# Kernel tuning notes

Hardware: AMD Instinct MI355X
Metric: run time of the kernel (lower is better)

The kernel has to match this reference:

```python
import jax, jax.numpy as jnp
import numpy as np

B, S, HID = 2, 1024, 2048
H, D, KV = 32, 64, 8          # query heads, head dim, kv heads (GQA)
INNER = H * D                 # 2048
KV_DIM = KV * D               # 512


def setup_inputs() -> dict:
    key = jax.random.key(0)
    ks = jax.random.split(key, 12)
    s = 0.02
    return {
        "query": jax.random.normal(ks[0], (B, S, HID), jnp.float32),
        "key": jax.random.normal(ks[1], (B, S, HID), jnp.float32),
        "value": jax.random.normal(ks[2], (B, S, HID), jnp.float32),
        "mask": jnp.zeros((B, 1, S, S), jnp.float32),
        "position_bias": jax.random.normal(ks[3], (1, H, S, S), jnp.float32),
        "Wq": jax.random.normal(ks[4], (HID, INNER), jnp.float32) * s,
        "bq": jnp.zeros((INNER,), jnp.float32),
        "Wk": jax.random.normal(ks[5], (HID, KV_DIM), jnp.float32) * s,
        "bk": jnp.zeros((KV_DIM,), jnp.float32),
        "Wv": jax.random.normal(ks[6], (HID, KV_DIM), jnp.float32) * s,
        "bv": jnp.zeros((KV_DIM,), jnp.float32),
        "Wo": jax.random.normal(ks[7], (INNER, HID), jnp.float32) * s,
        "bo": jnp.zeros((HID,), jnp.float32),
    }


def reference(query, key, value, mask, position_bias, Wq, bq, Wk, bk, Wv, bv, Wo, bo):
    # projections (torch nn.Linear equivalent, weights stored [in,out])
    q = (query @ Wq + bq).reshape(B, S, H, D)     # [B,S,H,D]
    k = (key @ Wk + bk).reshape(B, S, KV, D)      # [B,S,KV,D]
    v = (value @ Wv + bv).reshape(B, S, KV, D)
    rep = H // KV
    k = jnp.repeat(k, rep, axis=2)                # GQA repeat_kv -> [B,S,H,D]
    v = jnp.repeat(v, rep, axis=2)
    scores = jnp.einsum("bqhd,bkhd->bhqk", q, k)  # [B,H,S,S]
    scores = (scores + position_bias) * (1.0 / jnp.sqrt(jnp.float32(D)))
    scores = scores + mask
    probs = jax.nn.softmax(scores.astype(jnp.float32), axis=-1).astype(q.dtype)
    out = jnp.einsum("bhqk,bkhd->bqhd", probs, v).reshape(B, S, INNER)
    return out @ Wo + bo                          # [B,S,HID]
```

## Files before the change

### kernel.cpp

```cpp
#include <hip/hip_runtime.h>
#include <stdint.h>


#define DEVI __device__ __forceinline__

typedef __attribute__((ext_vector_type(8))) short bf16x8;
typedef __attribute__((ext_vector_type(4))) float f32x4;
typedef __attribute__((ext_vector_type(4))) float flt4;
typedef __attribute__((ext_vector_type(8))) unsigned short u16x8;
typedef __attribute__((ext_vector_type(4))) unsigned short u16x4;

DEVI unsigned short f2bf(float f){
  union{float f;uint32_t u;}v; v.f=f;
  uint32_t u=v.u;
  u += 0x7FFFu + ((u>>16)&1u);
  return (unsigned short)(u>>16);
}

DEVI uint32_t cvt_pk_bf16(float lo, float hi){
  uint32_t r;
  asm("v_cvt_pk_bf16_f32 %0, %1, %2" : "=v"(r) : "v"(lo), "v"(hi));
  return r;
}

DEVI float fexp2(float x){
#if __has_builtin(__builtin_amdgcn_exp2f)
  return __builtin_amdgcn_exp2f(x);
#else
  return exp2f(x);
#endif
}

DEVI void gload16(const void* g, void* l){
  __builtin_amdgcn_global_load_lds((const __attribute__((address_space(1))) void*)g,
                                   (__attribute__((address_space(3))) void*)l, 16, 0, 0);
}

__global__ void prep_k(const float* __restrict__ q, const float* __restrict__ k,
                       const float* __restrict__ v,
                       unsigned short* __restrict__ qb, unsigned short* __restrict__ kb,
                       unsigned short* __restrict__ vb,
                       const float* __restrict__ Wq, const float* __restrict__ Wk,
                       const float* __restrict__ Wv, const float* __restrict__ Wo,
                       unsigned short* __restrict__ WqT, unsigned short* __restrict__ WkT,
                       unsigned short* __restrict__ WvT, unsigned short* __restrict__ WoT){
  __shared__ float tile[64][65];
  int bid = blockIdx.x;
  if (bid < 6144){
    int z = bid>>11;
    int i = (bid&2047)*256 + threadIdx.x;
    const float* src = z==0 ? q : (z==1 ? k : v);
    unsigned short* dst = z==0 ? qb : (z==1 ? kb : vb);
    const flt4* s = (const flt4*)src;
    flt4 a = s[2*i], b = s[2*i+1];
    u16x8 o;
    o[0]=f2bf(a.x); o[1]=f2bf(a.y); o[2]=f2bf(a.z); o[3]=f2bf(a.w);
    o[4]=f2bf(b.x); o[5]=f2bf(b.y); o[6]=f2bf(b.z); o[7]=f2bf(b.w);
    ((u16x8*)dst)[i] = o;
    return;
  }
  int id = bid - 6144;
  const int K = 2048;
  const float* W; unsigned short* WT; int N, tt;
  if (id < 1024)      { W=Wq; WT=WqT; N=2048; tt=id; }
  else if (id < 1280) { W=Wk; WT=WkT; N=512;  tt=id-1024; }
  else if (id < 1536) { W=Wv; WT=WvT; N=512;  tt=id-1280; }
  else                { W=Wo; WT=WoT; N=2048; tt=id-1536; }
  int sh = (N==2048) ? 5 : 3;
  int n0 = (tt & ((1<<sh)-1))*64, k0 = (tt >> sh)*64;
  int t = threadIdx.x;
  int r = t>>4, c4 = (t&15)*4;
  #pragma unroll
  for (int i=0;i<4;i++){
    flt4 vv = *(const flt4*)&W[(size_t)(k0 + r + i*16)*N + n0 + c4];
    tile[r+i*16][c4+0]=vv.x; tile[r+i*16][c4+1]=vv.y; tile[r+i*16][c4+2]=vv.z; tile[r+i*16][c4+3]=vv.w;
  }
  __syncthreads();
  #pragma unroll
  for (int i=0;i<4;i++){
    int rn = r + i*16;
    u16x4 o;
    o[0]=f2bf(tile[c4+0][rn]); o[1]=f2bf(tile[c4+1][rn]);
    o[2]=f2bf(tile[c4+2][rn]); o[3]=f2bf(tile[c4+3][rn]);
    *(u16x4*)&WT[(size_t)(n0+rn)*K + k0 + c4] = o;
  }
}

#define GEMM64_KSTEP(A_, BT_, K_)                                              \
    __syncthreads();                                                           \
    _Pragma("unroll")                                                          \
    for (int j=0;j<2;j++){                                                     \
      int cid = (j*4+w)*64 + l;                                                \
      int row = cid>>3, sl = cid&7;                                            \
      int gsl = sl ^ (row&7);                                                  \
      gload16(&A_ [(size_t)(m0+row)*K_ + k0 + gsl*8], &As[(j*4+w)*512]);       \
      gload16(&BT_[(size_t)(n0+row)*K_ + k0 + gsl*8], &Bs[(j*4+w)*512]);       \
    }                                                                          \
    __syncthreads();                                                           \
    _Pragma("unroll")                                                          \
    for (int kk=0;kk<2;kk++){                                                  \
      bf16x8 af[2], bfv[2];                                                    \
      _Pragma("unroll")                                                        \
      for (int mt=0;mt<2;mt++){                                                \
        int row = wr+mt*16+lq;                                                 \
        af[mt] = *(const bf16x8*)&As[row*64 + (((kk*4+lg)^(lq&7))*8)];         \
      }                                                                        \
      _Pragma("unroll")                                                        \
      for (int nt=0;nt<2;nt++){                                                \
        int row = wc+nt*16+lq;                                                 \
        bfv[nt] = *(const bf16x8*)&Bs[row*64 + (((kk*4+lg)^(lq&7))*8)];        \
      }                                                                        \
      _Pragma("unroll")                                                        \
      for (int mt=0;mt<2;mt++)                                                 \
        _Pragma("unroll")                                                      \
        for (int nt=0;nt<2;nt++)                                               \
          acc[mt][nt] = __builtin_amdgcn_mfma_f32_16x16x32_bf16(af[mt], bfv[nt], acc[mt][nt], 0,0,0); \
    }

__global__ __launch_bounds__(256) void qkv64(const unsigned short* __restrict__ qbf,
    const unsigned short* __restrict__ kbf, const unsigned short* __restrict__ vbf,
    const unsigned short* __restrict__ WqT, const unsigned short* __restrict__ WkT,
    const unsigned short* __restrict__ WvT,
    const float* __restrict__ bq, const float* __restrict__ bk, const float* __restrict__ bv,
    unsigned short* __restrict__ Qp, unsigned short* __restrict__ Kp, unsigned short* __restrict__ VTb){
  __shared__ unsigned short As[64*64];
  __shared__ unsigned short Bs[64*64];
  const int K = 2048;
  int id = blockIdx.x;
  const unsigned short *A, *BT; const float* bias; int N, op, tt;
  if (id < 1024)      { op=0; A=qbf; BT=WqT; bias=bq; N=2048; tt=id; }
  else if (id < 1280) { op=1; A=kbf; BT=WkT; bias=bk; N=512;  tt=id-1024; }
  else                { op=2; A=vbf; BT=WvT; bias=bv; N=512;  tt=id-1280; }
  int sh = (N==2048) ? 5 : 3;
  int n0 = (tt & ((1<<sh)-1))*64, m0 = (tt >> sh)*64;
  int t = threadIdx.x, w = t>>6, l = t&63;
  int lq = l&15, lg = l>>4;
  int wr = (w>>1)*32, wc = (w&1)*32;
  f32x4 acc[2][2] = {};
  for (int k0=0;k0<K;k0+=64){
    GEMM64_KSTEP(A, BT, K)
  }
  #pragma unroll
  for (int nt=0;nt<2;nt++){
    int col = n0 + wc + nt*16 + lq;
    float bvl = bias[col];
    #pragma unroll
    for (int mt=0;mt<2;mt++){
      #pragma unroll
      for (int r=0;r<4;r++){
        int row = m0 + wr + mt*16 + lg*4 + r;
        float v = acc[mt][nt][r] + bvl;
        if (op==0)      Qp[(size_t)row*2048 + col] = f2bf(v);
        else if (op==1) Kp[(size_t)row*512 + col] = f2bf(v);
        else {
          int b = row>>10, s = row&1023;
          VTb[((size_t)(b*512 + col)<<10) + s] = f2bf(v);
        }
      }
    }
  }
}

__global__ __launch_bounds__(256) void oproj64(const unsigned short* __restrict__ A,
    const unsigned short* __restrict__ BT, const float* __restrict__ bias,
    float* __restrict__ Cout){
  __shared__ unsigned short As[64*64];
  __shared__ unsigned short Bs[64*64];
  const int K = 2048, N = 2048;
  int n0 = blockIdx.x*64, m0 = blockIdx.y*64;
  int t = threadIdx.x, w = t>>6, l = t&63;
  int lq = l&15, lg = l>>4;
  int wr = (w>>1)*32, wc = (w&1)*32;
  f32x4 acc[2][2] = {};
  for (int k0=0;k0<K;k0+=64){
    GEMM64_KSTEP(A, BT, K)
  }
  #pragma unroll
  for (int nt=0;nt<2;nt++){
    int col = n0 + wc + nt*16 + lq;
    float bvl = bias[col];
    #pragma unroll
    for (int mt=0;mt<2;mt++){
      #pragma unroll
      for (int r=0;r<4;r++){
        int row = m0 + wr + mt*16 + lg*4 + r;
        Cout[(size_t)row*N + col] = acc[mt][nt][r] + bvl;
      }
    }
  }
}

__global__ __launch_bounds__(512,2) void attn_k(const unsigned short* __restrict__ Q,
    const unsigned short* __restrict__ Kp, const unsigned short* __restrict__ VT,
    const float* __restrict__ pbias, const float* __restrict__ mask,
    unsigned short* __restrict__ Oout){
  __shared__ unsigned short Ks[2][2][2048];
  __shared__ unsigned short VTs[2][4096];
  __shared__ float Ms[2][2][1024];
  __shared__ unsigned short Pb[8][512];
  int t=threadIdx.x, w=t>>6, l=t&63;
  int kv = blockIdx.x & 7;
  int qb = blockIdx.x >> 3;
  int h = kv*4 + (w&3);
  int qhalf = w>>2;
  int lq = l&15, lg = l>>4;
  int q0 = qb*32 + qhalf*16;
  int mr = qhalf*16 + lq;
  bf16x8 qfA0, qfA1, qfB0, qfB1;
  {
    const unsigned short* qp = &Q[((size_t)(q0 + lq))*2048 + h*64 + lg*8];
    qfA0 = *(const bf16x8*)qp;  qfA1 = *(const bf16x8*)(qp + 32);
    qp += (size_t)1024*2048;
    qfB0 = *(const bf16x8*)qp;  qfB1 = *(const bf16x8*)(qp + 32);
  }
  const float* pbase = &pbias[((size_t)h*1024 + (q0+lq))*1024];
  f32x4 oaccA[4] = {}, oaccB[4] = {};
  float psumA = 0.f, psumB = 0.f;
  const float L2E   = 1.4426950408889634f;
  const float SCL2E = 0.125f*1.4426950408889634f;
  const float NFM   = -16.0f*1.4426950408889634f;
  unsigned short* pw = &Pb[w][0];
  int swz = (lq&3)<<3;

  flt4 RA[2], RB[2], comb[2][2];

#define ATTN_STAGE(buf_, kt_)                                                            \
  {                                                                                      \
    { int bb = w>>2; int row = (w&3)*8 + (l>>3); int ch = (l&7)^(row&7);                 \
      gload16(&Kp[((size_t)(bb*1024 + (kt_)*32 + row))*512 + kv*64 + ch*8],              \
              &Ks[buf_][0][0] + w*512); }                                                \
    { int row = w*8 + (l>>3); int g = (l&7)^(row&7);                                     \
      gload16(&VT[((size_t)((g>>2)*512 + kv*64 + row))*1024 + (kt_)*32 + (g&3)*8],       \
              &VTs[buf_][0] + w*512); }                                                  \
    { int bb = w>>2; int row = (w&3)*8 + (l>>3); int ch = (l&7)^(row&7);                 \
      gload16(&mask[((size_t)(bb*1024 + qb*32 + row))*1024 + (kt_)*32 + ch*4],           \
              &Ms[buf_][0][0] + w*256); }                                                \
  }

#define ATTN_RAW(RP_, kt_)                                                               \
  _Pragma("unroll")                                                                      \
  for (int nt=0;nt<2;nt++)                                                               \
    RP_[nt] = *(const flt4*)&pbase[(kt_)*32 + nt*16 + lg*4];

#define ATTN_COMBINE(RP_, cur_)                                                          \
  _Pragma("unroll")                                                                      \
  for (int bb=0;bb<2;bb++)                                                               \
    _Pragma("unroll")                                                                    \
    for (int nt=0;nt<2;nt++){                                                            \
      flt4 m4 = *(const flt4*)&Ms[cur_][bb][mr*32 + (((nt*4+lg)^(mr&7))<<2)];            \
      _Pragma("unroll")                                                                  \
      for (int r=0;r<4;r++)                                                              \
        comb[bb][nt][r] = fmaf(RP_[nt][r], SCL2E, fmaf(m4[r], L2E, NFM));                \
    }

#define COMPUTE_BATCH(P_, bb_, QF0_, QF1_, OACC_, PS_)                                   \
  {                                                                                      \
    f32x4 sacc[2] = {};                                                                  \
    __builtin_amdgcn_s_setprio(1);                                                       \
    _Pragma("unroll")                                                                    \
    for (int nt=0;nt<2;nt++){                                                            \
      int row = nt*16 + lq;                                                              \
      bf16x8 kf0 = *(const bf16x8*)&Ks[P_][bb_][row*64 + (( lg    ^ (row&7))*8)];        \
      bf16x8 kf1 = *(const bf16x8*)&Ks[P_][bb_][row*64 + (((4+lg) ^ (row&7))*8)];        \
      sacc[nt] = __builtin_amdgcn_mfma_f32_16x16x32_bf16(kf0, QF0_, sacc[nt], 0,0,0);    \
      sacc[nt] = __builtin_amdgcn_mfma_f32_16x16x32_bf16(kf1, QF1_, sacc[nt], 0,0,0);    \
    }                                                                                    \
    __builtin_amdgcn_s_setprio(0);                                                       \
    _Pragma("unroll")                                                                    \
    for (int nt=0;nt<2;nt++){                                                            \
      float p0 = fexp2(fmaf(sacc[nt][0], SCL2E, comb[bb_][nt][0]));                      \
      float p1 = fexp2(fmaf(sacc[nt][1], SCL2E, comb[bb_][nt][1]));                      \
      float p2 = fexp2(fmaf(sacc[nt][2], SCL2E, comb[bb_][nt][2]));                      \
      float p3 = fexp2(fmaf(sacc[nt][3], SCL2E, comb[bb_][nt][3]));                      \
      PS_ += (p0+p1)+(p2+p3);                                                            \
      uint2 pk;                                                                          \
      pk.x = cvt_pk_bf16(p0,p1);                                                         \
      pk.y = cvt_pk_bf16(p2,p3);                                                         \
      *(uint2*)&pw[lq*32 + ((nt*16 + lg*4) ^ swz)] = pk;                                 \
    }                                                                                    \
    {                                                                                    \
      bf16x8 pa = *(const bf16x8*)&pw[lq*32 + ((lg*8) ^ swz)];                           \
      __builtin_amdgcn_s_setprio(1);                                                     \
      _Pragma("unroll")                                                                  \
      for (int nt=0;nt<4;nt++){                                                          \
        int vrow = nt*16 + lq;                                                           \
        bf16x8 vf = *(const bf16x8*)&VTs[P_][vrow*64 + ((((bb_)*4+lg) ^ (vrow&7))*8)];   \
        OACC_[nt] = __builtin_amdgcn_mfma_f32_16x16x32_bf16(pa, vf, OACC_[nt], 0,0,0);   \
      }                                                                                  \
      __builtin_amdgcn_s_setprio(0);                                                     \
    }                                                                                    \
  }

#define TILE(kt_, cur_, RP_, DOSTAGE, DORAW, VMFULL)                                     \
  {                                                                                      \
    if (DOSTAGE) ATTN_STAGE((cur_)^1, (kt_)+1)                                           \
    if (VMFULL) { asm volatile("s_waitcnt vmcnt(5)" ::: "memory"); }                     \
    else        { asm volatile("s_waitcnt vmcnt(0)" ::: "memory"); }                     \
    __builtin_amdgcn_s_barrier();                                                        \
    ATTN_COMBINE(RP_, cur_)                                                              \
    if (DORAW) ATTN_RAW(RP_, (kt_)+2)                                                    \
    COMPUTE_BATCH(cur_, 0, qfA0, qfA1, oaccA, psumA)                                     \
    COMPUTE_BATCH(cur_, 1, qfB0, qfB1, oaccB, psumB)                                     \
    __builtin_amdgcn_s_barrier();                                                        \
  }

  ATTN_STAGE(0, 0)
  ATTN_RAW(RA, 0)
  ATTN_RAW(RB, 1)

  for (int kb=0; kb<30; kb+=2){
    TILE(kb+0, 0, RA, 1, 1, 1)
    TILE(kb+1, 1, RB, 1, 1, 1)
  }
  TILE(30, 0, RA, 1, 0, 1)
  TILE(31, 1, RB, 0, 0, 0)

  {
    float lsum = psumA;
    lsum += __shfl_xor(lsum, 16);
    lsum += __shfl_xor(lsum, 32);
    #pragma unroll
    for (int r=0;r<4;r++){
      float lr = __shfl(lsum, lg*4 + r);
      float linv = 1.f/lr;
      int qrow = q0 + lg*4 + r;
      #pragma unroll
      for (int nt=0;nt<4;nt++)
        Oout[((size_t)qrow)*2048 + h*64 + nt*16 + lq] = f2bf(oaccA[nt][r]*linv);
    }
  }
  {
    float lsum = psumB;
    lsum += __shfl_xor(lsum, 16);
    lsum += __shfl_xor(lsum, 32);
    #pragma unroll
    for (int r=0;r<4;r++){
      float lr = __shfl(lsum, lg*4 + r);
      float linv = 1.f/lr;
      int qrow = q0 + lg*4 + r;
      #pragma unroll
      for (int nt=0;nt<4;nt++)
        Oout[((size_t)(1024 + qrow))*2048 + h*64 + nt*16 + lq] = f2bf(oaccB[nt][r]*linv);
    }
  }
#undef TILE
#undef COMPUTE_BATCH
#undef ATTN_COMBINE
#undef ATTN_RAW
#undef ATTN_STAGE
}

extern "C" void kernel_launch(void* const* d_in, const int* in_sizes, int n_in,
                              void* d_out, int out_size, void* d_ws, size_t ws_size,
                              hipStream_t stream){
  (void)in_sizes; (void)n_in; (void)out_size; (void)ws_size;
  const float* query = (const float*)d_in[0];
  const float* key   = (const float*)d_in[1];
  const float* value = (const float*)d_in[2];
  const float* mask  = (const float*)d_in[3];
  const float* pbias = (const float*)d_in[4];
  const float* Wq = (const float*)d_in[5];
  const float* bq = (const float*)d_in[6];
  const float* Wk = (const float*)d_in[7];
  const float* bk = (const float*)d_in[8];
  const float* Wv = (const float*)d_in[9];
  const float* bv = (const float*)d_in[10];
  const float* Wo = (const float*)d_in[11];
  const float* bo = (const float*)d_in[12];
  char* ws = (char*)d_ws;
  const size_t MB = (size_t)1<<20;
  unsigned short* qbf = (unsigned short*)(ws + 0*MB);
  unsigned short* kbf = (unsigned short*)(ws + 8*MB);
  unsigned short* vbf = (unsigned short*)(ws + 16*MB);
  unsigned short* WqT = (unsigned short*)(ws + 24*MB);
  unsigned short* WkT = (unsigned short*)(ws + 32*MB);
  unsigned short* WvT = (unsigned short*)(ws + 34*MB);
  unsigned short* WoT = (unsigned short*)(ws + 36*MB);
  unsigned short* Qp  = (unsigned short*)(ws + 44*MB);
  unsigned short* Kp  = (unsigned short*)(ws + 52*MB);
  unsigned short* VTb = (unsigned short*)(ws + 54*MB);
  unsigned short* Aout= (unsigned short*)(ws + 56*MB);

  prep_k<<<8704,256,0,stream>>>(query, key, value, qbf, kbf, vbf,
                                Wq, Wk, Wv, Wo, WqT, WkT, WvT, WoT);
  qkv64<<<1536,256,0,stream>>>(qbf, kbf, vbf, WqT, WkT, WvT, bq, bk, bv, Qp, Kp, VTb);
  attn_k<<<256,512,0,stream>>>(Qp, Kp, VTb, pbias, mask, Aout);
  oproj64<<<dim3(32,32),256,0,stream>>>(Aout, WoT, bo, (float*)d_out);
}
```

Baseline: 151.0 us.

## Split attention work across batch per wave and stage position bias through LDS

Each attention block now covers 16 query rows for both batches: waves are split by batch instead of by query half, and each wave holds one Q fragment and one accumulator set instead of two. The grid doubles to 512 blocks and launch bounds ask for 4 blocks per CU, aiming for higher occupancy and lower register pressure. Position bias is now loaded asynchronously into swizzled LDS alongside K, V and mask, replacing per-thread direct global loads held two tiles ahead. The cost is that each K/V tile is reloaded by twice as many blocks, and the loop is simpler with less register prefetch.

```diff
diff --git a/kernel.cpp b/kernel.cpp
--- a/kernel.cpp
+++ b/kernel.cpp
@@ -190,89 +190,89 @@
   }
 }
 
-__global__ __launch_bounds__(512,2) void attn_k(const unsigned short* __restrict__ Q,
+__global__ __launch_bounds__(512,4) void attn_k(const unsigned short* __restrict__ Q,
     const unsigned short* __restrict__ Kp, const unsigned short* __restrict__ VT,
     const float* __restrict__ pbias, const float* __restrict__ mask,
     unsigned short* __restrict__ Oout){
   __shared__ unsigned short Ks[2][2][2048];
-  __shared__ unsigned short VTs[2][4096];
-  __shared__ float Ms[2][2][1024];
+  __shared__ unsigned short VTs[2][2][2048];
+  __shared__ float Ms[2][1024];
+  __shared__ float Bi[2][2048];
   __shared__ unsigned short Pb[8][512];
   int t=threadIdx.x, w=t>>6, l=t&63;
   int kv = blockIdx.x & 7;
   int qb = blockIdx.x >> 3;
-  int h = kv*4 + (w&3);
-  int qhalf = w>>2;
+  int bb = w>>2, h = kv*4 + (w&3);
   int lq = l&15, lg = l>>4;
-  int q0 = qb*32 + qhalf*16;
-  int mr = qhalf*16 + lq;
-  bf16x8 qfA0, qfA1, qfB0, qfB1;
+  int q0 = qb*16;
+  bf16x8 qf0, qf1;
   {
-    const unsigned short* qp = &Q[((size_t)(q0 + lq))*2048 + h*64 + lg*8];
-    qfA0 = *(const bf16x8*)qp;  qfA1 = *(const bf16x8*)(qp + 32);
-    qp += (size_t)1024*2048;
-    qfB0 = *(const bf16x8*)qp;  qfB1 = *(const bf16x8*)(qp + 32);
-  }
-  const float* pbase = &pbias[((size_t)h*1024 + (q0+lq))*1024];
-  f32x4 oaccA[4] = {}, oaccB[4] = {};
-  float psumA = 0.f, psumB = 0.f;
+    const unsigned short* qp = &Q[((size_t)(bb*1024 + q0 + lq))*2048 + h*64 + lg*8];
+    qf0 = *(const bf16x8*)qp;
+    qf1 = *(const bf16x8*)(qp + 32);
+  }
+  f32x4 oacc[4] = {};
+  float psum = 0.f;
   const float L2E   = 1.4426950408889634f;
   const float SCL2E = 0.125f*1.4426950408889634f;
   const float NFM   = -16.0f*1.4426950408889634f;
   unsigned short* pw = &Pb[w][0];
   int swz = (lq&3)<<3;
-
-  flt4 RA[2], RB[2], comb[2][2];
+  int rb = (w&3)*16 + lq;
+  int rm = bb*16 + lq;
+  flt4 comb[2];
 
 #define ATTN_STAGE(buf_, kt_)                                                            \
   {                                                                                      \
-    { int bb = w>>2; int row = (w&3)*8 + (l>>3); int ch = (l&7)^(row&7);                 \
-      gload16(&Kp[((size_t)(bb*1024 + (kt_)*32 + row))*512 + kv*64 + ch*8],              \
+    { int c = w*64 + l;  int cb = c>>8, r = (c>>3)&31, ch = c&7;                         \
+      gload16(&Kp[((size_t)(cb*1024 + (kt_)*32 + r))*512 + kv*64 + ((ch^(r&7))*8)],      \
               &Ks[buf_][0][0] + w*512); }                                                \
-    { int row = w*8 + (l>>3); int g = (l&7)^(row&7);                                     \
-      gload16(&VT[((size_t)((g>>2)*512 + kv*64 + row))*1024 + (kt_)*32 + (g&3)*8],       \
-              &VTs[buf_][0] + w*512); }                                                  \
-    { int bb = w>>2; int row = (w&3)*8 + (l>>3); int ch = (l&7)^(row&7);                 \
-      gload16(&mask[((size_t)(bb*1024 + qb*32 + row))*1024 + (kt_)*32 + ch*4],           \
-              &Ms[buf_][0][0] + w*256); }                                                \
-  }
-
-#define ATTN_RAW(RP_, kt_)                                                               \
+    { int c = w*64 + l;  int cb = c>>8, d = (c>>2)&63, ch = c&3;                         \
+      gload16(&VT[((size_t)(cb*512 + kv*64 + d))*1024 + (kt_)*32 + ((ch^(d&3))*8)],      \
+              &VTs[buf_][0][0] + w*512); }                                               \
+    { int c = w*64 + l;  int r6 = c>>3, ch = c&7;                                        \
+      gload16(&pbias[((size_t)((kv*4 + (r6>>4))*1024) + q0 + (r6&15))*1024               \
+                     + (kt_)*32 + ((ch^(r6&7))*4)],                                      \
+              &Bi[buf_][0] + w*256); }                                                   \
+    if (l < 32){                                                                         \
+      int c = w*32 + l;  int r5 = c>>3, ch = c&7;                                        \
+      gload16(&mask[((size_t)((r5>>4)*1024 + q0 + (r5&15)))*1024 + (kt_)*32              \
+                    + ((ch^(r5&7))*4)],                                                  \
+              &Ms[buf_][0] + w*128);                                                     \
+    }                                                                                    \
+  }
+
+#define ATTN_COMBINE(cur_)                                                               \
   _Pragma("unroll")                                                                      \
-  for (int nt=0;nt<2;nt++)                                                               \
-    RP_[nt] = *(const flt4*)&pbase[(kt_)*32 + nt*16 + lg*4];
-
-#define ATTN_COMBINE(RP_, cur_)                                                          \
-  _Pragma("unroll")                                                                      \
-  for (int bb=0;bb<2;bb++)                                                               \
+  for (int nt=0;nt<2;nt++){                                                              \
+    int j = nt*4 + lg;                                                                   \
+    flt4 b4 = *(const flt4*)&Bi[cur_][rb*32 + ((j^(rb&7))<<2)];                          \
+    flt4 m4 = *(const flt4*)&Ms[cur_][rm*32 + ((j^(rm&7))<<2)];                          \
     _Pragma("unroll")                                                                    \
-    for (int nt=0;nt<2;nt++){                                                            \
-      flt4 m4 = *(const flt4*)&Ms[cur_][bb][mr*32 + (((nt*4+lg)^(mr&7))<<2)];            \
-      _Pragma("unroll")                                                                  \
-      for (int r=0;r<4;r++)                                                              \
-        comb[bb][nt][r] = fmaf(RP_[nt][r], SCL2E, fmaf(m4[r], L2E, NFM));                \
-    }
-
-#define COMPUTE_BATCH(P_, bb_, QF0_, QF1_, OACC_, PS_)                                   \
+    for (int r=0;r<4;r++)                                                                \
+      comb[nt][r] = fmaf(b4[r], SCL2E, fmaf(m4[r], L2E, NFM));                           \
+  }
+
+#define ATTN_COMPUTE(P_)                                                                 \
   {                                                                                      \
     f32x4 sacc[2] = {};                                                                  \
     __builtin_amdgcn_s_setprio(1);                                                       \
     _Pragma("unroll")                                                                    \
     for (int nt=0;nt<2;nt++){                                                            \
-      int row = nt*16 + lq;                                                              \
-      bf16x8 kf0 = *(const bf16x8*)&Ks[P_][bb_][row*64 + (( lg    ^ (row&7))*8)];        \
-      bf16x8 kf1 = *(const bf16x8*)&Ks[P_][bb_][row*64 + (((4+lg) ^ (row&7))*8)];        \
-      sacc[nt] = __builtin_amdgcn_mfma_f32_16x16x32_bf16(kf0, QF0_, sacc[nt], 0,0,0);    \
-      sacc[nt] = __builtin_amdgcn_mfma_f32_16x16x32_bf16(kf1, QF1_, sacc[nt], 0,0,0);    \
+      int key = nt*16 + lq;                                                              \
+      bf16x8 kf0 = *(const bf16x8*)&Ks[P_][bb][key*64 + (( lg    ^ (key&7))*8)];         \
+      bf16x8 kf1 = *(const bf16x8*)&Ks[P_][bb][key*64 + (((4+lg) ^ (key&7))*8)];         \
+      sacc[nt] = __builtin_amdgcn_mfma_f32_16x16x32_bf16(kf0, qf0, sacc[nt], 0,0,0);     \
+      sacc[nt] = __builtin_amdgcn_mfma_f32_16x16x32_bf16(kf1, qf1, sacc[nt], 0,0,0);     \
     }                                                                                    \
     __builtin_amdgcn_s_setprio(0);                                                       \
     _Pragma("unroll")                                                                    \
     for (int nt=0;nt<2;nt++){                                                            \
-      float p0 = fexp2(fmaf(sacc[nt][0], SCL2E, comb[bb_][nt][0]));                      \
-      float p1 = fexp2(fmaf(sacc[nt][1], SCL2E, comb[bb_][nt][1]));                      \
-      float p2 = fexp2(fmaf(sacc[nt][2], SCL2E, comb[bb_][nt][2]));                      \
-      float p3 = fexp2(fmaf(sacc[nt][3], SCL2E, comb[bb_][nt][3]));                      \
-      PS_ += (p0+p1)+(p2+p3);                                                            \
+      float p0 = fexp2(fmaf(sacc[nt][0], SCL2E, comb[nt][0]));                           \
+      float p1 = fexp2(fmaf(sacc[nt][1], SCL2E, comb[nt][1]));                           \
+      float p2 = fexp2(fmaf(sacc[nt][2], SCL2E, comb[nt][2]));                           \
+      float p3 = fexp2(fmaf(sacc[nt][3], SCL2E, comb[nt][3]));                           \
+      psum += (p0+p1)+(p2+p3);                                                           \
       uint2 pk;                                                                          \
       pk.x = cvt_pk_bf16(p0,p1);                                                         \
       pk.y = cvt_pk_bf16(p2,p3);                                                         \
@@ -284,69 +284,44 @@
       _Pragma("unroll")                                                                  \
       for (int nt=0;nt<4;nt++){                                                          \
         int vrow = nt*16 + lq;                                                           \
-        bf16x8 vf = *(const bf16x8*)&VTs[P_][vrow*64 + ((((bb_)*4+lg) ^ (vrow&7))*8)];   \
-        OACC_[nt] = __builtin_amdgcn_mfma_f32_16x16x32_bf16(pa, vf, OACC_[nt], 0,0,0);   \
+        bf16x8 vf = *(const bf16x8*)&VTs[P_][bb][vrow*32 + ((lg ^ (vrow&3))*8)];         \
+        oacc[nt] = __builtin_amdgcn_mfma_f32_16x16x32_bf16(pa, vf, oacc[nt], 0,0,0);     \
       }                                                                                  \
       __builtin_amdgcn_s_setprio(0);                                                     \
     }                                                                                    \
   }
 
-#define TILE(kt_, cur_, RP_, DOSTAGE, DORAW, VMFULL)                                     \
-  {                                                                                      \
-    if (DOSTAGE) ATTN_STAGE((cur_)^1, (kt_)+1)                                           \
-    if (VMFULL) { asm volatile("s_waitcnt vmcnt(5)" ::: "memory"); }                     \
-    else        { asm volatile("s_waitcnt vmcnt(0)" ::: "memory"); }                     \
-    __builtin_amdgcn_s_barrier();                                                        \
-    ATTN_COMBINE(RP_, cur_)                                                              \
-    if (DORAW) ATTN_RAW(RP_, (kt_)+2)                                                    \
-    COMPUTE_BATCH(cur_, 0, qfA0, qfA1, oaccA, psumA)                                     \
-    COMPUTE_BATCH(cur_, 1, qfB0, qfB1, oaccB, psumB)                                     \
-    __builtin_amdgcn_s_barrier();                                                        \
-  }
-
   ATTN_STAGE(0, 0)
-  ATTN_RAW(RA, 0)
-  ATTN_RAW(RB, 1)
-
-  for (int kb=0; kb<30; kb+=2){
-    TILE(kb+0, 0, RA, 1, 1, 1)
-    TILE(kb+1, 1, RB, 1, 1, 1)
-  }
-  TILE(30, 0, RA, 1, 0, 1)
-  TILE(31, 1, RB, 0, 0, 0)
-
-  {
-    float lsum = psumA;
-    lsum += __shfl_xor(lsum, 16);
-    lsum += __shfl_xor(lsum, 32);
+
+  for (int kt=0; kt<32; ++kt){
+    int cur = kt&1;
+    if (kt < 31){
+      ATTN_STAGE(cur^1, kt+1)
+      asm volatile("s_waitcnt vmcnt(4)" ::: "memory");
+    } else {
+      asm volatile("s_waitcnt vmcnt(0)" ::: "memory");
+    }
+    __builtin_amdgcn_s_barrier();
+    ATTN_COMBINE(cur)
+    ATTN_COMPUTE(cur)
+    __builtin_amdgcn_s_barrier();
+  }
+
+  float lsum = psum;
+  lsum += __shfl_xor(lsum, 16);
+  lsum += __shfl_xor(lsum, 32);
+  #pragma unroll
+  for (int r=0;r<4;r++){
+    float lr = __shfl(lsum, lg*4 + r);
+    float linv = 1.f/lr;
+    int qrow = q0 + lg*4 + r;
     #pragma unroll
-    for (int r=0;r<4;r++){
-      float lr = __shfl(lsum, lg*4 + r);
-      float linv = 1.f/lr;
-      int qrow = q0 + lg*4 + r;
-      #pragma unroll
-      for (int nt=0;nt<4;nt++)
-        Oout[((size_t)qrow)*2048 + h*64 + nt*16 + lq] = f2bf(oaccA[nt][r]*linv);
-    }
-  }
-  {
-    float lsum = psumB;
-    lsum += __shfl_xor(lsum, 16);
-    lsum += __shfl_xor(lsum, 32);
-    #pragma unroll
-    for (int r=0;r<4;r++){
-      float lr = __shfl(lsum, lg*4 + r);
-      float linv = 1.f/lr;
-      int qrow = q0 + lg*4 + r;
-      #pragma unroll
-      for (int nt=0;nt<4;nt++)
-        Oout[((size_t)(1024 + qrow))*2048 + h*64 + nt*16 + lq] = f2bf(oaccB[nt][r]*linv);
-    }
-  }
-#undef TILE
-#undef COMPUTE_BATCH
+    for (int nt=0;nt<4;nt++){
+      Oout[((size_t)(bb*1024 + qrow))*2048 + h*64 + nt*16 + lq] = f2bf(oacc[nt][r]*linv);
+    }
+  }
+#undef ATTN_COMPUTE
 #undef ATTN_COMBINE
-#undef ATTN_RAW
 #undef ATTN_STAGE
 }
 
@@ -384,6 +359,6 @@
   prep_k<<<8704,256,0,stream>>>(query, key, value, qbf, kbf, vbf,
                                 Wq, Wk, Wv, Wo, WqT, WkT, WvT, WoT);
   qkv64<<<1536,256,0,stream>>>(qbf, kbf, vbf, WqT, WkT, WvT, bq, bk, bv, Qp, Kp, VTb);
-  attn_k<<<256,512,0,stream>>>(Qp, Kp, VTb, pbias, mask, Aout);
+  attn_k<<<512,512,0,stream>>>(Qp, Kp, VTb, pbias, mask, Aout);
   oproj64<<<dim3(32,32),256,0,stream>>>(Aout, WoT, bo, (float*)d_out);
 }
```

After: 155.4 us. +2.9%, slower.
